# Performance work log

Measured on AMD Instinct MI355X. Metric: run time of the kernel, lower is better.

Reference implementation:

```python
import jax, jax.numpy as jnp
import numpy as np

B, L, A, F = 4096, 12, 768, 4096  # batch, n_layers, d_activations, d_features


def setup_inputs() -> dict:
    key = jax.random.key(0)
    k_x, k_enc, k_dec, k_m, k_s = jax.random.split(key, 5)
    x = jax.random.normal(k_x, (B, L, A), dtype=jnp.float32)
    # Encoder: uniform(-1/sqrt(F), 1/sqrt(F)) per reset_parameters
    enc_thresh = 1.0 / np.sqrt(F)
    W_enc = jax.random.uniform(k_enc, (L, A, F), jnp.float32, -enc_thresh, enc_thresh)
    # Decoder: triangular weights W_i of shape (i+1, F, A), packed along axis 0.
    # Total rows = L*(L+1)//2. uniform(-1/sqrt(A*L), 1/sqrt(A*L)).
    dec_thresh = 1.0 / np.sqrt(A * L)
    n_tri = L * (L + 1) // 2
    W_dec_packed = jax.random.uniform(k_dec, (n_tri, F, A), jnp.float32, -dec_thresh, dec_thresh)
    # JumpReLU threshold per (layer, feature), init 0.03
    theta = jnp.full((L, F), 0.03, dtype=jnp.float32)
    # Dimensionwise input standardizer stats (per layer, per activation dim)
    in_mean = 0.1 * jax.random.normal(k_m, (L, A), dtype=jnp.float32)
    in_std = 1.0 + 0.1 * jax.random.uniform(k_s, (L, A), dtype=jnp.float32)
    return {"x": x, "in_mean": in_mean, "in_std": in_std, "W_enc": W_enc,
            "theta": theta, "W_dec_packed": W_dec_packed}


def reference(x, in_mean, in_std, W_enc, theta, W_dec_packed):
    # Input standardization: (x - mean) / std, broadcast over batch
    sx = (x - in_mean[None]) / in_std[None]                      # [B, L, A]
    # Encoder: per-layer dense projection
    enc = jnp.einsum('bla,laf->blf', sx, W_enc)                  # [B, L, F]
    # JumpReLU: x * (x > theta)
    act = enc * (enc > theta[None]).astype(enc.dtype)            # [B, L, F]
    # Decoder: triangular accumulation. Layer i reads features of layers 0..i
    # with its own weight tensor W_i (slice of the packed triangular buffer).
    n_layers = W_enc.shape[0]
    preds = []
    off = 0
    for i in range(n_layers):
        W_i = W_dec_packed[off:off + i + 1]                      # [i+1, F, A]
        preds.append(jnp.einsum('blf,lfa->ba', act[:, :i + 1], W_i))
        off += i + 1
    logits = jnp.stack(preds, axis=1)                            # [B, L, A]
    # Original forward returns (logits, encoder_out, concat_w_dec); the
    # concat_w_dec list is just a reshape of the decoder params, omitted here.
    return logits, enc
```

## Files before the change

### kernel.cpp

```cpp
#include <hip/hip_runtime.h>
#include <cstdint>
#include <cstddef>

#define B_ 4096
#define L_ 12
#define A_ 768
#define F_ 4096
#define NTRI 78

typedef __bf16 bf16x8 __attribute__((ext_vector_type(8)));
typedef float f32x4 __attribute__((ext_vector_type(4)));
typedef unsigned short u16x4 __attribute__((ext_vector_type(4)));
typedef unsigned short u16x8 __attribute__((ext_vector_type(8)));

__device__ __forceinline__ unsigned short f32_to_bf16(float f) {
  unsigned int u = __float_as_uint(f);
  u += 0x7fffu + ((u >> 16) & 1u);
  return (unsigned short)(u >> 16);
}

__device__ __forceinline__ void gload_lds16(const void* g, void* l) {
  __builtin_amdgcn_global_load_lds(
      (const __attribute__((address_space(1))) void*)g,
      (__attribute__((address_space(3))) void*)l,
      16, 0, 0);
}

__global__ __launch_bounds__(256) void prep_sx(
    const float* __restrict__ x, const float* __restrict__ mean,
    const float* __restrict__ stdv, unsigned short* __restrict__ sx) {
  size_t i4 = (size_t)blockIdx.x * 256 + threadIdx.x;
  size_t e = i4 * 4;
  if (e >= (size_t)B_ * L_ * A_) return;
  unsigned int a = (unsigned int)(e % A_);
  unsigned int t = (unsigned int)(e / A_);
  unsigned int b = t / L_;
  unsigned int l = t % L_;
  float4 xv = *(const float4*)(x + e);
  float4 mv = *(const float4*)(mean + (size_t)l * A_ + a);
  float4 sv = *(const float4*)(stdv + (size_t)l * A_ + a);
  u16x4 o;
  o.x = f32_to_bf16((xv.x - mv.x) / sv.x);
  o.y = f32_to_bf16((xv.y - mv.y) / sv.y);
  o.z = f32_to_bf16((xv.z - mv.z) / sv.z);
  o.w = f32_to_bf16((xv.w - mv.w) / sv.w);
  *(u16x4*)(sx + ((size_t)l * B_ + b) * A_ + a) = o;
}

__global__ __launch_bounds__(256) void transpose_cvt64(
    const float* __restrict__ in, unsigned short* __restrict__ out,
    int R, int C) {
  __shared__ float tile[64][65];
  const float* inz = in + (size_t)blockIdx.z * R * C;
  unsigned short* outz = out + (size_t)blockIdx.z * R * C;
  const int c0 = blockIdx.x * 64, r0 = blockIdx.y * 64;
  const int t = threadIdx.x;
  {
    const int c = (t & 15) * 4;
    const int rb = t >> 4;
#pragma unroll
    for (int q = 0; q < 4; ++q) {
      const int r = rb + q * 16;
      float4 v = *(const float4*)(inz + (size_t)(r0 + r) * C + (c0 + c));
      tile[r][c] = v.x; tile[r][c + 1] = v.y;
      tile[r][c + 2] = v.z; tile[r][c + 3] = v.w;
    }
  }
  __syncthreads();
  {
    const int c = t >> 2;
    const int rb = (t & 3) * 16;
#pragma unroll
    for (int h = 0; h < 2; ++h) {
      u16x8 o;
#pragma unroll
      for (int j = 0; j < 8; ++j) o[j] = f32_to_bf16(tile[rb + h * 8 + j][c]);
      *(u16x8*)(outz + (size_t)(c0 + c) * R + (r0 + rb + h * 8)) = o;
    }
  }
}

template <class KOffA, class KOffB>
__device__ __forceinline__ void gemm_core64(
    int KT, char* AS, char* BS,
    const char* gA0, const char* gB0, int ldA, int ldB,
    int w, int wr, int wc, int lane,
    KOffA koffA, KOffB koffB, f32x4 (&acc)[8][4]) {
  const int g = lane >> 4;
  const int fr = lane & 15;
  const int f7 = fr & 7;
  const uint32_t aRow = (uint32_t)(wr * 128 + fr) * 128;
  const uint32_t bRow = (uint32_t)(wc * 64 + fr) * 128;
  const uint32_t c0 = (uint32_t)((g ^ f7) * 16);
  const uint32_t c1 = (uint32_t)(((4 | g) ^ f7) * 16);
  const uint32_t aOff0 = aRow + c0, aOff1 = aRow + c1;
  const uint32_t bOff0 = bRow + c0, bOff1 = bRow + c1;

  auto stageA = [&](int kt) {
    uint32_t off = koffA(kt);
    char* d = AS + ((kt & 1) << 15) + (w << 10);
#pragma unroll
    for (int q = 0; q < 4; ++q)
      gload_lds16(gA0 + off + (uint32_t)q * 64u * (uint32_t)ldA, d + q * 8192);
  };
  auto stageB = [&](int kt) {
    uint32_t off = koffB(kt);
    char* d = BS + ((kt & 1) << 15) + (w << 10);
#pragma unroll
    for (int q = 0; q < 4; ++q)
      gload_lds16(gB0 + off + (uint32_t)q * 64u * (uint32_t)ldB, d + q * 8192);
  };

  stageA(0);
  stageB(0);
  asm volatile("s_waitcnt vmcnt(0)" ::: "memory");
  __builtin_amdgcn_s_barrier();

  bf16x8 bk[4], aA[4], aB[4];
  for (int kt = 0; kt < KT; ++kt) {
    const char* Ab = AS + ((kt & 1) << 15);
    const char* Bb = BS + ((kt & 1) << 15);
    const bool more = (kt + 1 < KT);
#pragma unroll
    for (int ni = 0; ni < 4; ++ni)
      bk[ni] = *(const bf16x8*)(Bb + bOff0 + ni * 2048);
#pragma unroll
    for (int mi = 0; mi < 4; ++mi)
      aA[mi] = *(const bf16x8*)(Ab + aOff0 + mi * 2048);
    if (more) stageA(kt + 1);
    asm volatile("" ::: "memory");
    __builtin_amdgcn_s_barrier();
    __builtin_amdgcn_s_setprio(1);
#pragma unroll
    for (int mi = 0; mi < 4; ++mi)
#pragma unroll
      for (int ni = 0; ni < 4; ++ni)
        acc[mi][ni] = __builtin_amdgcn_mfma_f32_16x16x32_bf16(
            aA[mi], bk[ni], acc[mi][ni], 0, 0, 0);
    __builtin_amdgcn_s_setprio(0);
    asm volatile("" ::: "memory");
    __builtin_amdgcn_s_barrier();
#pragma unroll
    for (int mi = 0; mi < 4; ++mi)
      aB[mi] = *(const bf16x8*)(Ab + aOff0 + (4 + mi) * 2048);
    if (more) stageB(kt + 1);
    asm volatile("" ::: "memory");
    __builtin_amdgcn_s_barrier();
    __builtin_amdgcn_s_setprio(1);
#pragma unroll
    for (int mi = 0; mi < 4; ++mi)
#pragma unroll
      for (int ni = 0; ni < 4; ++ni)
        acc[mi + 4][ni] = __builtin_amdgcn_mfma_f32_16x16x32_bf16(
            aB[mi], bk[ni], acc[mi + 4][ni], 0, 0, 0);
    __builtin_amdgcn_s_setprio(0);
    asm volatile("" ::: "memory");
    __builtin_amdgcn_s_barrier();
#pragma unroll
    for (int ni = 0; ni < 4; ++ni)
      bk[ni] = *(const bf16x8*)(Bb + bOff1 + ni * 2048);
#pragma unroll
    for (int mi = 0; mi < 4; ++mi)
      aA[mi] = *(const bf16x8*)(Ab + aOff1 + mi * 2048);
    asm volatile("" ::: "memory");
    __builtin_amdgcn_s_barrier();
    __builtin_amdgcn_s_setprio(1);
#pragma unroll
    for (int mi = 0; mi < 4; ++mi)
#pragma unroll
      for (int ni = 0; ni < 4; ++ni)
        acc[mi][ni] = __builtin_amdgcn_mfma_f32_16x16x32_bf16(
            aA[mi], bk[ni], acc[mi][ni], 0, 0, 0);
    __builtin_amdgcn_s_setprio(0);
    asm volatile("" ::: "memory");
    __builtin_amdgcn_s_barrier();
#pragma unroll
    for (int mi = 0; mi < 4; ++mi)
      aB[mi] = *(const bf16x8*)(Ab + aOff1 + (4 + mi) * 2048);
    asm volatile("" ::: "memory");
    __builtin_amdgcn_s_barrier();
    __builtin_amdgcn_s_setprio(1);
#pragma unroll
    for (int mi = 0; mi < 4; ++mi)
#pragma unroll
      for (int ni = 0; ni < 4; ++ni)
        acc[mi + 4][ni] = __builtin_amdgcn_mfma_f32_16x16x32_bf16(
            aB[mi], bk[ni], acc[mi + 4][ni], 0, 0, 0);
    __builtin_amdgcn_s_setprio(0);
    asm volatile("s_waitcnt vmcnt(0)" ::: "memory");
    __builtin_amdgcn_s_barrier();
  }
}

__global__ __launch_bounds__(512, 2) void enc_gemm8(
    const unsigned short* __restrict__ sxT,
    const unsigned short* __restrict__ wT,
    const float* __restrict__ theta,
    float* __restrict__ enc_out,
    unsigned short* __restrict__ act)
{
  extern __shared__ __align__(16) char lds[];
  char* AS = lds;
  char* BS = lds + 65536;
  const int b = blockIdx.x;
  const int wg = (b & 7) * 384 + (b >> 3);
  const int l = wg >> 8;
  const int blk = wg & 255;
  const int m0 = (blk & 15) * 256;
  const int n0 = (blk >> 4) * 256;
  const int tid = threadIdx.x;
  const int w = tid >> 6, lane = tid & 63;
  const int wr = w >> 2, wc = w & 3;
  const int sg = (lane & 7) ^ (lane >> 3);
  const int srow = w * 8 + (lane >> 3);

  const char* gA0 = (const char*)sxT +
      ((size_t)l * B_ + m0 + srow) * (A_ * 2) + sg * 16;
  const char* gB0 = (const char*)wT +
      ((size_t)l * F_ + n0 + srow) * (A_ * 2) + sg * 16;

  f32x4 acc[8][4] = {};
  auto koffA = [](int kt) { return (uint32_t)kt * 128u; };
  auto koffB = [](int kt) { return (uint32_t)kt * 128u; };
  gemm_core64(A_ / 64, AS, BS, gA0, gB0, A_ * 2, A_ * 2, w, wr, wc, lane,
              koffA, koffB, acc);

  const int g = lane >> 4, fr = lane & 15;
#pragma unroll
  for (int ni = 0; ni < 4; ++ni) {
    const int gcol = n0 + wc * 64 + ni * 16 + fr;
    const float th = theta[(size_t)l * F_ + gcol];
#pragma unroll
    for (int mi = 0; mi < 8; ++mi) {
      const int growb = m0 + wr * 128 + mi * 16 + g * 4;
#pragma unroll
      for (int jj = 0; jj < 4; ++jj) {
        const float v = acc[mi][ni][jj];
        const size_t grow = (size_t)(growb + jj);
        enc_out[(grow * L_ + l) * F_ + gcol] = v;
        act[((size_t)l * B_ + grow) * F_ + gcol] =
            (v > th) ? f32_to_bf16(v) : (unsigned short)0;
      }
    }
  }
}

__global__ __launch_bounds__(512, 2) void dec_gemm8(
    const unsigned short* __restrict__ act,
    const unsigned short* __restrict__ wdecT,
    float* __restrict__ logits)
{
  extern __shared__ __align__(16) char lds[];
  char* AS = lds;
  char* BS = lds + 65536;
  const int b = blockIdx.x;
  const int z = b / 48;
  const int blk = b - z * 48;
  const int i = 11 - z;
  const int m0 = (blk & 15) * 256;
  const int n0 = (blk >> 4) * 256;
  const int triBase = i * (i + 1) / 2;
  const int KT = (i + 1) * 64;
  const int tid = threadIdx.x;
  const int w = tid >> 6, lane = tid & 63;
  const int wr = w >> 2, wc = w & 3;
  const int sg = (lane & 7) ^ (lane >> 3);
  const int srow = w * 8 + (lane >> 3);

  const char* gA0 = (const char*)act + ((size_t)(m0 + srow)) * (F_ * 2) + sg * 16;
  const char* gB0 = (const char*)wdecT +
      ((size_t)(triBase * A_ + n0 + srow)) * (F_ * 2) + sg * 16;

  f32x4 acc[8][4] = {};
  auto koffA = [](int kt) {
    return (uint32_t)(kt >> 6) * (uint32_t)(B_ * F_ * 2) +
           (uint32_t)(kt & 63) * 128u;
  };
  auto koffB = [](int kt) {
    return (uint32_t)(kt >> 6) * (uint32_t)(A_ * F_ * 2) +
           (uint32_t)(kt & 63) * 128u;
  };
  gemm_core64(KT, AS, BS, gA0, gB0, F_ * 2, F_ * 2, w, wr, wc, lane,
              koffA, koffB, acc);

  const int g = lane >> 4, fr = lane & 15;
#pragma unroll
  for (int mi = 0; mi < 8; ++mi) {
    const int growb = m0 + wr * 128 + mi * 16 + g * 4;
#pragma unroll
    for (int ni = 0; ni < 4; ++ni) {
      const int gcol = n0 + wc * 64 + ni * 16 + fr;
#pragma unroll
      for (int jj = 0; jj < 4; ++jj)
        logits[((size_t)(growb + jj) * L_ + i) * A_ + gcol] = acc[mi][ni][jj];
    }
  }
}

extern "C" void kernel_launch(void* const* d_in, const int* in_sizes, int n_in,
                              void* d_out, int out_size, void* d_ws,
                              size_t ws_size, hipStream_t stream) {
  (void)in_sizes; (void)n_in; (void)out_size; (void)ws_size;
  const float* x = (const float*)d_in[0];
  const float* mean = (const float*)d_in[1];
  const float* stdv = (const float*)d_in[2];
  const float* Wenc = (const float*)d_in[3];
  const float* theta = (const float*)d_in[4];
  const float* Wdec = (const float*)d_in[5];

  float* logits = (float*)d_out;
  float* enc = (float*)d_out + (size_t)B_ * L_ * A_;

  char* ws = (char*)d_ws;
  const size_t actBytes = (size_t)L_ * B_ * F_ * 2;
  const size_t sxBytes = (size_t)L_ * B_ * A_ * 2;
  unsigned short* act = (unsigned short*)ws;
  unsigned short* sx = (unsigned short*)(ws + actBytes);
  unsigned short* wencT = (unsigned short*)(ws + actBytes + sxBytes);
  unsigned short* wdecT = (unsigned short*)(ws + actBytes);

  hipFuncSetAttribute((const void*)enc_gemm8,
                      hipFuncAttributeMaxDynamicSharedMemorySize, 131072);
  hipFuncSetAttribute((const void*)dec_gemm8,
                      hipFuncAttributeMaxDynamicSharedMemorySize, 131072);

  prep_sx<<<(B_ * L_ * A_ / 4 + 255) / 256, 256, 0, stream>>>(x, mean, stdv, sx);
  transpose_cvt64<<<dim3(F_ / 64, A_ / 64, L_), 256, 0, stream>>>(
      Wenc, wencT, A_, F_);
  enc_gemm8<<<3072, 512, 131072, stream>>>(sx, wencT, theta, enc, act);
  transpose_cvt64<<<dim3(A_ / 64, F_ / 64, NTRI), 256, 0, stream>>>(
      Wdec, wdecT, F_, A_);
  dec_gemm8<<<576, 512, 131072, stream>>>(act, wdecT, logits);
}
```

Measured before the change: 2.826 ms.

## Split K-tile staging into two halves with finer-grained vmcnt waits

Each 64-wide K tile is now staged into LDS as two 32-wide halves, each with its own row layout and 4-way XOR swizzle. Prefetch of the next tile's second half is issued mid-iteration, and partial s_waitcnt vmcnt(4) lets compute on the first half start before the second half lands. The aim is better overlap of global-to-LDS loads with MFMA work and fewer full-drain stalls. The cost is more complex wait accounting, and the new swizzle may bring different LDS bank-conflict behaviour.

```diff
diff --git a/kernel.cpp b/kernel.cpp
--- a/kernel.cpp
+++ b/kernel.cpp
@@ -88,32 +88,32 @@
     KOffA koffA, KOffB koffB, f32x4 (&acc)[8][4]) {
   const int g = lane >> 4;
   const int fr = lane & 15;
-  const int f7 = fr & 7;
-  const uint32_t aRow = (uint32_t)(wr * 128 + fr) * 128;
-  const uint32_t bRow = (uint32_t)(wc * 64 + fr) * 128;
-  const uint32_t c0 = (uint32_t)((g ^ f7) * 16);
-  const uint32_t c1 = (uint32_t)(((4 | g) ^ f7) * 16);
-  const uint32_t aOff0 = aRow + c0, aOff1 = aRow + c1;
-  const uint32_t bOff0 = bRow + c0, bOff1 = bRow + c1;
-
-  auto stageA = [&](int kt) {
-    uint32_t off = koffA(kt);
-    char* d = AS + ((kt & 1) << 15) + (w << 10);
-#pragma unroll
-    for (int q = 0; q < 4; ++q)
-      gload_lds16(gA0 + off + (uint32_t)q * 64u * (uint32_t)ldA, d + q * 8192);
+  const uint32_t swz = (uint32_t)((g ^ (fr & 3)) * 16);
+  const uint32_t aBase = (uint32_t)(wr * 128 + fr) * 64 + swz;
+  const uint32_t bBase = (uint32_t)(wc * 64 + fr) * 64 + swz;
+
+  auto stageA = [&](int kt, int h) {
+    const uint32_t off = koffA(kt) + (uint32_t)(h * 64);
+    char* d = AS + ((kt & 1) << 15) + (h << 14) + (w << 10);
+#pragma unroll
+    for (int q = 0; q < 2; ++q)
+      gload_lds16(gA0 + off + (uint32_t)((q * 8 + w) * 16) * (uint32_t)ldA,
+                  d + q * 8192);
   };
-  auto stageB = [&](int kt) {
-    uint32_t off = koffB(kt);
-    char* d = BS + ((kt & 1) << 15) + (w << 10);
-#pragma unroll
-    for (int q = 0; q < 4; ++q)
-      gload_lds16(gB0 + off + (uint32_t)q * 64u * (uint32_t)ldB, d + q * 8192);
+  auto stageB = [&](int kt, int h) {
+    const uint32_t off = koffB(kt) + (uint32_t)(h * 64);
+    char* d = BS + ((kt & 1) << 15) + (h << 14) + (w << 10);
+#pragma unroll
+    for (int q = 0; q < 2; ++q)
+      gload_lds16(gB0 + off + (uint32_t)((q * 8 + w) * 16) * (uint32_t)ldB,
+                  d + q * 8192);
   };
 
-  stageA(0);
-  stageB(0);
-  asm volatile("s_waitcnt vmcnt(0)" ::: "memory");
+  stageA(0, 0);
+  stageB(0, 0);
+  stageA(0, 1);
+  stageB(0, 1);
+  asm volatile("s_waitcnt vmcnt(4)" ::: "memory");
   __builtin_amdgcn_s_barrier();
 
   bf16x8 bk[4], aA[4], aB[4];
@@ -123,11 +123,11 @@
     const bool more = (kt + 1 < KT);
 #pragma unroll
     for (int ni = 0; ni < 4; ++ni)
-      bk[ni] = *(const bf16x8*)(Bb + bOff0 + ni * 2048);
-#pragma unroll
-    for (int mi = 0; mi < 4; ++mi)
-      aA[mi] = *(const bf16x8*)(Ab + aOff0 + mi * 2048);
-    if (more) stageA(kt + 1);
+      bk[ni] = *(const bf16x8*)(Bb + bBase + ni * 1024);
+#pragma unroll
+    for (int mi = 0; mi < 4; ++mi)
+      aA[mi] = *(const bf16x8*)(Ab + aBase + mi * 1024);
+    if (more) stageA(kt + 1, 0);
     asm volatile("" ::: "memory");
     __builtin_amdgcn_s_barrier();
     __builtin_amdgcn_s_setprio(1);
@@ -142,8 +142,8 @@
     __builtin_amdgcn_s_barrier();
 #pragma unroll
     for (int mi = 0; mi < 4; ++mi)
-      aB[mi] = *(const bf16x8*)(Ab + aOff0 + (4 + mi) * 2048);
-    if (more) stageB(kt + 1);
+      aB[mi] = *(const bf16x8*)(Ab + aBase + (4 + mi) * 1024);
+    if (more) stageB(kt + 1, 0);
     asm volatile("" ::: "memory");
     __builtin_amdgcn_s_barrier();
     __builtin_amdgcn_s_setprio(1);
@@ -154,14 +154,16 @@
         acc[mi + 4][ni] = __builtin_amdgcn_mfma_f32_16x16x32_bf16(
             aB[mi], bk[ni], acc[mi + 4][ni], 0, 0, 0);
     __builtin_amdgcn_s_setprio(0);
-    asm volatile("" ::: "memory");
+    if (more) { asm volatile("s_waitcnt vmcnt(4)" ::: "memory"); }
+    else      { asm volatile("s_waitcnt vmcnt(0)" ::: "memory"); }
     __builtin_amdgcn_s_barrier();
 #pragma unroll
     for (int ni = 0; ni < 4; ++ni)
-      bk[ni] = *(const bf16x8*)(Bb + bOff1 + ni * 2048);
-#pragma unroll
-    for (int mi = 0; mi < 4; ++mi)
-      aA[mi] = *(const bf16x8*)(Ab + aOff1 + mi * 2048);
+      bk[ni] = *(const bf16x8*)(Bb + 16384 + bBase + ni * 1024);
+#pragma unroll
+    for (int mi = 0; mi < 4; ++mi)
+      aA[mi] = *(const bf16x8*)(Ab + 16384 + aBase + mi * 1024);
+    if (more) stageA(kt + 1, 1);
     asm volatile("" ::: "memory");
     __builtin_amdgcn_s_barrier();
     __builtin_amdgcn_s_setprio(1);
@@ -176,7 +178,8 @@
     __builtin_amdgcn_s_barrier();
 #pragma unroll
     for (int mi = 0; mi < 4; ++mi)
-      aB[mi] = *(const bf16x8*)(Ab + aOff1 + (4 + mi) * 2048);
+      aB[mi] = *(const bf16x8*)(Ab + 16384 + aBase + (4 + mi) * 1024);
+    if (more) stageB(kt + 1, 1);
     asm volatile("" ::: "memory");
     __builtin_amdgcn_s_barrier();
     __builtin_amdgcn_s_setprio(1);
@@ -187,7 +190,7 @@
         acc[mi + 4][ni] = __builtin_amdgcn_mfma_f32_16x16x32_bf16(
             aB[mi], bk[ni], acc[mi + 4][ni], 0, 0, 0);
     __builtin_amdgcn_s_setprio(0);
-    asm volatile("s_waitcnt vmcnt(0)" ::: "memory");
+    if (more) { asm volatile("s_waitcnt vmcnt(4)" ::: "memory"); }
     __builtin_amdgcn_s_barrier();
   }
 }
@@ -211,13 +214,13 @@
   const int tid = threadIdx.x;
   const int w = tid >> 6, lane = tid & 63;
   const int wr = w >> 2, wc = w & 3;
-  const int sg = (lane & 7) ^ (lane >> 3);
-  const int srow = w * 8 + (lane >> 3);
+  const int srow2 = lane >> 2;
+  const int scol2 = ((lane & 3) ^ (srow2 & 3)) * 16;
 
   const char* gA0 = (const char*)sxT +
-      ((size_t)l * B_ + m0 + srow) * (A_ * 2) + sg * 16;
+      ((size_t)l * B_ + m0 + srow2) * (A_ * 2) + scol2;
   const char* gB0 = (const char*)wT +
-      ((size_t)l * F_ + n0 + srow) * (A_ * 2) + sg * 16;
+      ((size_t)l * F_ + n0 + srow2) * (A_ * 2) + scol2;
 
   f32x4 acc[8][4] = {};
   auto koffA = [](int kt) { return (uint32_t)kt * 128u; };
@@ -264,12 +267,13 @@
   const int tid = threadIdx.x;
   const int w = tid >> 6, lane = tid & 63;
   const int wr = w >> 2, wc = w & 3;
-  const int sg = (lane & 7) ^ (lane >> 3);
-  const int srow = w * 8 + (lane >> 3);
-
-  const char* gA0 = (const char*)act + ((size_t)(m0 + srow)) * (F_ * 2) + sg * 16;
+  const int srow2 = lane >> 2;
+  const int scol2 = ((lane & 3) ^ (srow2 & 3)) * 16;
+
+  const char* gA0 =
+      (const char*)act + ((size_t)(m0 + srow2)) * (F_ * 2) + scol2;
   const char* gB0 = (const char*)wdecT +
-      ((size_t)(triBase * A_ + n0 + srow)) * (F_ * 2) + sg * 16;
+      ((size_t)(triBase * A_ + n0 + srow2)) * (F_ * 2) + scol2;
 
   f32x4 acc[8][4] = {};
   auto koffA = [](int kt) {
```

Result: slower. 2.984 ms (+5.6%).

## Switch GEMM core to K=32 tiles with four-stage LDS prefetch pipeline

Applied to the files above, without the earlier changes.

The shared GEMM core now uses 32-wide K tiles instead of 64-wide ones. It keeps four LDS buffers and prefetches three stages ahead, waiting with partial vmcnt counts rather than draining all loads every iteration. The swizzle and staging addresses are rebuilt to match the 64-byte rows. The aim is to hide global-load latency better across iterations. In exchange there are twice as many iterations and barriers per K, and the vmcnt bookkeeping is more fragile.

```diff
diff --git a/kernel.cpp b/kernel.cpp
--- a/kernel.cpp
+++ b/kernel.cpp
@@ -81,53 +81,49 @@
 }
 
 template <class KOffA, class KOffB>
-__device__ __forceinline__ void gemm_core64(
+__device__ __forceinline__ void gemm_core32(
     int KT, char* AS, char* BS,
-    const char* gA0, const char* gB0, int ldA, int ldB,
+    const char* gA0s, const char* gB0s,
+    int ldA, int ldB,
     int w, int wr, int wc, int lane,
     KOffA koffA, KOffB koffB, f32x4 (&acc)[8][4]) {
   const int g = lane >> 4;
   const int fr = lane & 15;
-  const int f7 = fr & 7;
-  const uint32_t aRow = (uint32_t)(wr * 128 + fr) * 128;
-  const uint32_t bRow = (uint32_t)(wc * 64 + fr) * 128;
-  const uint32_t c0 = (uint32_t)((g ^ f7) * 16);
-  const uint32_t c1 = (uint32_t)(((4 | g) ^ f7) * 16);
-  const uint32_t aOff0 = aRow + c0, aOff1 = aRow + c1;
-  const uint32_t bOff0 = bRow + c0, bOff1 = bRow + c1;
+  const uint32_t ssr = (uint32_t)((g ^ ((fr >> 1) & 3)) * 16);
+  const uint32_t aBase = (uint32_t)(wr * 128 + fr) * 64 + ssr;
+  const uint32_t bBase = (uint32_t)(wc * 64 + fr) * 64 + ssr;
 
   auto stageA = [&](int kt) {
-    uint32_t off = koffA(kt);
-    char* d = AS + ((kt & 1) << 15) + (w << 10);
-#pragma unroll
-    for (int q = 0; q < 4; ++q)
-      gload_lds16(gA0 + off + (uint32_t)q * 64u * (uint32_t)ldA, d + q * 8192);
+    const uint32_t off = koffA(kt);
+    char* d = AS + (kt & 3) * 16384 + (w << 10);
+    gload_lds16(gA0s + off, d);
+    gload_lds16(gA0s + off + 128u * (uint32_t)ldA, d + 8192);
   };
   auto stageB = [&](int kt) {
-    uint32_t off = koffB(kt);
-    char* d = BS + ((kt & 1) << 15) + (w << 10);
-#pragma unroll
-    for (int q = 0; q < 4; ++q)
-      gload_lds16(gB0 + off + (uint32_t)q * 64u * (uint32_t)ldB, d + q * 8192);
+    const uint32_t off = koffB(kt);
+    char* d = BS + (kt & 3) * 16384 + (w << 10);
+    gload_lds16(gB0s + off, d);
+    gload_lds16(gB0s + off + 128u * (uint32_t)ldB, d + 8192);
   };
 
-  stageA(0);
-  stageB(0);
-  asm volatile("s_waitcnt vmcnt(0)" ::: "memory");
+  stageA(0); stageB(0);
+  stageA(1); stageB(1);
+  stageA(2); stageB(2);
+  asm volatile("s_waitcnt vmcnt(8)" ::: "memory");
   __builtin_amdgcn_s_barrier();
 
   bf16x8 bk[4], aA[4], aB[4];
   for (int kt = 0; kt < KT; ++kt) {
-    const char* Ab = AS + ((kt & 1) << 15);
-    const char* Bb = BS + ((kt & 1) << 15);
-    const bool more = (kt + 1 < KT);
+    const char* Ab = AS + (kt & 3) * 16384;
+    const char* Bb = BS + (kt & 3) * 16384;
+    const bool more = (kt + 3 < KT);
 #pragma unroll
     for (int ni = 0; ni < 4; ++ni)
-      bk[ni] = *(const bf16x8*)(Bb + bOff0 + ni * 2048);
+      bk[ni] = *(const bf16x8*)(Bb + bBase + ni * 1024);
 #pragma unroll
     for (int mi = 0; mi < 4; ++mi)
-      aA[mi] = *(const bf16x8*)(Ab + aOff0 + mi * 2048);
-    if (more) stageA(kt + 1);
+      aA[mi] = *(const bf16x8*)(Ab + aBase + mi * 1024);
+    if (more) stageA(kt + 3);
     asm volatile("" ::: "memory");
     __builtin_amdgcn_s_barrier();
     __builtin_amdgcn_s_setprio(1);
@@ -142,8 +138,8 @@
     __builtin_amdgcn_s_barrier();
 #pragma unroll
     for (int mi = 0; mi < 4; ++mi)
-      aB[mi] = *(const bf16x8*)(Ab + aOff0 + (4 + mi) * 2048);
-    if (more) stageB(kt + 1);
+      aB[mi] = *(const bf16x8*)(Ab + aBase + (4 + mi) * 1024);
+    if (more) stageB(kt + 3);
     asm volatile("" ::: "memory");
     __builtin_amdgcn_s_barrier();
     __builtin_amdgcn_s_setprio(1);
@@ -154,40 +150,9 @@
         acc[mi + 4][ni] = __builtin_amdgcn_mfma_f32_16x16x32_bf16(
             aB[mi], bk[ni], acc[mi + 4][ni], 0, 0, 0);
     __builtin_amdgcn_s_setprio(0);
-    asm volatile("" ::: "memory");
-    __builtin_amdgcn_s_barrier();
-#pragma unroll
-    for (int ni = 0; ni < 4; ++ni)
-      bk[ni] = *(const bf16x8*)(Bb + bOff1 + ni * 2048);
-#pragma unroll
-    for (int mi = 0; mi < 4; ++mi)
-      aA[mi] = *(const bf16x8*)(Ab + aOff1 + mi * 2048);
-    asm volatile("" ::: "memory");
-    __builtin_amdgcn_s_barrier();
-    __builtin_amdgcn_s_setprio(1);
-#pragma unroll
-    for (int mi = 0; mi < 4; ++mi)
-#pragma unroll
-      for (int ni = 0; ni < 4; ++ni)
-        acc[mi][ni] = __builtin_amdgcn_mfma_f32_16x16x32_bf16(
-            aA[mi], bk[ni], acc[mi][ni], 0, 0, 0);
-    __builtin_amdgcn_s_setprio(0);
-    asm volatile("" ::: "memory");
-    __builtin_amdgcn_s_barrier();
-#pragma unroll
-    for (int mi = 0; mi < 4; ++mi)
-      aB[mi] = *(const bf16x8*)(Ab + aOff1 + (4 + mi) * 2048);
-    asm volatile("" ::: "memory");
-    __builtin_amdgcn_s_barrier();
-    __builtin_amdgcn_s_setprio(1);
-#pragma unroll
-    for (int mi = 0; mi < 4; ++mi)
-#pragma unroll
-      for (int ni = 0; ni < 4; ++ni)
-        acc[mi + 4][ni] = __builtin_amdgcn_mfma_f32_16x16x32_bf16(
-            aB[mi], bk[ni], acc[mi + 4][ni], 0, 0, 0);
-    __builtin_amdgcn_s_setprio(0);
-    asm volatile("s_waitcnt vmcnt(0)" ::: "memory");
+    if (more)                { asm volatile("s_waitcnt vmcnt(8)" ::: "memory"); }
+    else if (kt + 2 < KT)    { asm volatile("s_waitcnt vmcnt(4)" ::: "memory"); }
+    else if (kt + 1 < KT)    { asm volatile("s_waitcnt vmcnt(0)" ::: "memory"); }
     __builtin_amdgcn_s_barrier();
   }
 }
@@ -211,18 +176,18 @@
   const int tid = threadIdx.x;
   const int w = tid >> 6, lane = tid & 63;
   const int wr = w >> 2, wc = w & 3;
-  const int sg = (lane & 7) ^ (lane >> 3);
-  const int srow = w * 8 + (lane >> 3);
-
-  const char* gA0 = (const char*)sxT +
-      ((size_t)l * B_ + m0 + srow) * (A_ * 2) + sg * 16;
-  const char* gB0 = (const char*)wT +
-      ((size_t)l * F_ + n0 + srow) * (A_ * 2) + sg * 16;
+  const int srowS = w * 16 + (lane >> 2);
+  const int chnkS = ((lane & 3) ^ ((lane >> 3) & 3)) * 16;
+
+  const char* gA0s = (const char*)sxT +
+      ((size_t)l * B_ + m0 + srowS) * (A_ * 2) + chnkS;
+  const char* gB0s = (const char*)wT +
+      ((size_t)l * F_ + n0 + srowS) * (A_ * 2) + chnkS;
 
   f32x4 acc[8][4] = {};
-  auto koffA = [](int kt) { return (uint32_t)kt * 128u; };
-  auto koffB = [](int kt) { return (uint32_t)kt * 128u; };
-  gemm_core64(A_ / 64, AS, BS, gA0, gB0, A_ * 2, A_ * 2, w, wr, wc, lane,
+  auto koffA = [](int kt) { return (uint32_t)kt * 64u; };
+  auto koffB = [](int kt) { return (uint32_t)kt * 64u; };
+  gemm_core32(A_ / 32, AS, BS, gA0s, gB0s, A_ * 2, A_ * 2, w, wr, wc, lane,
               koffA, koffB, acc);
 
   const int g = lane >> 4, fr = lane & 15;
@@ -260,27 +225,28 @@
   const int m0 = (blk & 15) * 256;
   const int n0 = (blk >> 4) * 256;
   const int triBase = i * (i + 1) / 2;
-  const int KT = (i + 1) * 64;
+  const int KT = (i + 1) * 128;
   const int tid = threadIdx.x;
   const int w = tid >> 6, lane = tid & 63;
   const int wr = w >> 2, wc = w & 3;
-  const int sg = (lane & 7) ^ (lane >> 3);
-  const int srow = w * 8 + (lane >> 3);
-
-  const char* gA0 = (const char*)act + ((size_t)(m0 + srow)) * (F_ * 2) + sg * 16;
-  const char* gB0 = (const char*)wdecT +
-      ((size_t)(triBase * A_ + n0 + srow)) * (F_ * 2) + sg * 16;
+  const int srowS = w * 16 + (lane >> 2);
+  const int chnkS = ((lane & 3) ^ ((lane >> 3) & 3)) * 16;
+
+  const char* gA0s =
+      (const char*)act + ((size_t)(m0 + srowS)) * (F_ * 2) + chnkS;
+  const char* gB0s = (const char*)wdecT +
+      ((size_t)(triBase * A_ + n0 + srowS)) * (F_ * 2) + chnkS;
 
   f32x4 acc[8][4] = {};
   auto koffA = [](int kt) {
-    return (uint32_t)(kt >> 6) * (uint32_t)(B_ * F_ * 2) +
-           (uint32_t)(kt & 63) * 128u;
+    return (uint32_t)(kt >> 7) * (uint32_t)(B_ * F_ * 2) +
+           (uint32_t)(kt & 127) * 64u;
   };
   auto koffB = [](int kt) {
-    return (uint32_t)(kt >> 6) * (uint32_t)(A_ * F_ * 2) +
-           (uint32_t)(kt & 63) * 128u;
+    return (uint32_t)(kt >> 7) * (uint32_t)(A_ * F_ * 2) +
+           (uint32_t)(kt & 127) * 64u;
   };
-  gemm_core64(KT, AS, BS, gA0, gB0, F_ * 2, F_ * 2, w, wr, wc, lane,
+  gemm_core32(KT, AS, BS, gA0s, gB0s, F_ * 2, F_ * 2, w, wr, wc, lane,
               koffA, koffB, acc);
 
   const int g = lane >> 4, fr = lane & 15;
```

New measurement: 2.940 ms. +4.1%, slower.
